# Performance work log

Hardware: AMD Instinct MI355X
Metric: run time of the kernel (lower is better)

Reference implementation:

```python
import jax, jax.numpy as jnp
import numpy as np
from jax import lax

COCO_80_TO_91 = [1,2,3,4,5,6,7,8,9,10,11,13,14,15,16,17,18,19,20,21,22,23,24,25,27,28,31,32,33,34,35,36,37,38,39,40,41,42,43,44,46,47,48,49,50,51,52,53,54,55,56,57,58,59,60,61,62,63,64,65,67,70,72,73,74,75,76,77,78,79,80,81,82,84,85,86,87,88,89,90]

CONF = 0.25      # self.confidence
IOU_THR = 0.7    # ultralytics NMS default
TOPK = 1000      # candidate cap before NMS
MAX_DET = 300    # ultralytics max_det default
MAX_WH = 7680.0  # per-class offset trick
IMG_SZ = 640.0   # yolov8 letterboxed input size


def setup_inputs() -> dict:
    key = jax.random.key(0)
    preds = jax.random.uniform(key, (32, 84, 8400), dtype=jnp.float32)
    return {"preds": preds}


def _nms_single(boxes, scores):
    """Greedy NMS on score-descending boxes [K,4] (class-offset xyxy). Returns keep mask [K]."""
    K = boxes.shape[0]
    area = (boxes[:, 2] - boxes[:, 0]) * (boxes[:, 3] - boxes[:, 1])  # [K]
    lt = jnp.maximum(boxes[:, None, :2], boxes[None, :, :2])          # [K,K,2]
    rb = jnp.minimum(boxes[:, None, 2:], boxes[None, :, 2:])
    wh = jnp.clip(rb - lt, 0.0)
    inter = wh[..., 0] * wh[..., 1]
    iou = inter / (area[:, None] + area[None, :] - inter + 1e-7)       # [K,K]
    idx = jnp.arange(K)
    sup = (iou > IOU_THR) & (idx[None, :] > idx[:, None])              # i suppresses later j

    def body(i, keep):
        return jnp.where(keep[i], keep & ~sup[i], keep)

    return lax.fori_loop(0, K, body, jnp.ones((K,), dtype=bool))


def reference(preds):
    # preds: [B, 84, N] -> [B, N, 84]
    p = jnp.transpose(preds, (0, 2, 1))
    box_xywh = p[..., :4] * IMG_SZ           # xywh in pixels on 640x640 canvas
    cls = p[..., 4:]                          # [B, N, 80]
    scores = jnp.max(cls, axis=-1)            # best-class confidence
    labels = jnp.argmax(cls, axis=-1)         # 0..79
    xy, wh = box_xywh[..., :2], box_xywh[..., 2:]
    xyxy = jnp.concatenate([xy - wh * 0.5, xy + wh * 0.5], axis=-1)  # decode

    # confidence filter + top-K candidate selection (score-descending)
    s_masked = jnp.where(scores > CONF, scores, -1.0)
    top_s, top_i = lax.top_k(s_masked, TOPK)                          # [B,TOPK]
    top_b = jnp.take_along_axis(xyxy, top_i[..., None], axis=1)      # [B,TOPK,4]
    top_l = jnp.take_along_axis(labels, top_i, axis=1)               # [B,TOPK]

    # per-class NMS via class offset
    off_b = top_b + (top_l.astype(top_b.dtype) * MAX_WH)[..., None]
    keep = jax.vmap(_nms_single)(off_b, top_s) & (top_s > CONF)

    # select final max_det detections, zero-pad invalid slots
    fin_s = jnp.where(keep, top_s, -1.0)
    out_s, out_i = lax.top_k(fin_s, MAX_DET)                          # [B,MAX_DET]
    out_b = jnp.take_along_axis(top_b, out_i[..., None], axis=1)
    out_l = jnp.take_along_axis(top_l, out_i, axis=1)
    valid = out_s > CONF
    boxes = jnp.where(valid[..., None], out_b, 0.0)
    scores_out = jnp.where(valid, out_s, 0.0)
    mapped = jnp.asarray(COCO_80_TO_91, dtype=jnp.int64)[out_l]       # COCO 80 -> 91 ids
    labels_out = jnp.where(valid, mapped, 0)
    return boxes, scores_out, labels_out
```

## Files before the change

### kernel.cpp

```cpp
#include <hip/hip_runtime.h>
#include <stdint.h>

typedef unsigned long long u64;
typedef unsigned int u32;

#define BATCH 32
#define NCH 84
#define NA 8400
#define NCLS 80
#define TOPK 1000
#define MAXDET 300
#define CONF 0.25f
#define IOU_T 0.7f
#define MAX_WH 7680.0f
#define IMG_SZ 640.0f
#define NT 1024
#define KPT 9
#define NCOPY 8
#define HPAD 260
#define DTILE 256

__device__ __constant__ float coco_map_f[NCLS] = {
    1,2,3,4,5,6,7,8,9,10,11,13,14,15,16,17,18,19,20,21,22,23,24,25,27,28,
    31,32,33,34,35,36,37,38,39,40,41,42,43,44,46,47,48,49,50,51,52,53,54,
    55,56,57,58,59,60,61,62,63,64,65,67,70,72,73,74,75,76,77,78,79,80,81,
    82,84,85,86,87,88,89,90};

__device__ inline u64 shflx64(u64 v, int m) {
    int lo = __shfl_xor((int)(u32)(v & 0xFFFFFFFFull), m, 64);
    int hi = __shfl_xor((int)(u32)(v >> 32), m, 64);
    return ((u64)(u32)hi << 32) | (u32)lo;
}

__global__ __launch_bounds__(256)
void decode_kernel(const float* __restrict__ preds,
                   u64* __restrict__ keys,
                   float4* __restrict__ boxes) {
    const int b = blockIdx.y;
    const int t = threadIdx.x;
    const int w = t >> 6, l = t & 63;
    const int wa = blockIdx.x * DTILE + w * 64;
    const int a = wa + l;
    const float* p = preds + (size_t)b * NCH * NA;

    __shared__ float stage[4][16][64];

    float bx = 0.f, by = 0.f, bw = 0.f, bh = 0.f;
    float best = -1.0f;
    int bl = 0;

    const int rsel = l >> 4;
    const int c4 = (l & 15) * 4;
    const int col = wa + c4;

    for (int chunk = 0; chunk < 6; ++chunk) {
        const int r0 = chunk * 16;
        const int nq = (chunk == 5) ? 1 : 4;
        for (int i = 0; i < nq; ++i) {
            int row = r0 + i * 4 + rsel;
            float4 v = (col < NA) ? *(const float4*)(p + (size_t)row * NA + col)
                                  : make_float4(0.f, 0.f, 0.f, 0.f);
            *(float4*)&stage[w][i * 4 + rsel][c4] = v;
        }
        __builtin_amdgcn_s_waitcnt(0xc07f);
        const int nr = (chunk == 5) ? 4 : 16;
        if (chunk == 0) {
            bx = stage[w][0][l]; by = stage[w][1][l];
            bw = stage[w][2][l]; bh = stage[w][3][l];
            best = stage[w][4][l]; bl = 0;
            for (int r = 5; r < 16; ++r) {
                float v = stage[w][r][l];
                int c = r - 4;
                bl = (v > best) ? c : bl;  best = fmaxf(v, best);
            }
        } else {
            for (int r = 0; r < nr; ++r) {
                float v = stage[w][r][l];
                int c = r0 + r - 4;
                bl = (v > best) ? c : bl;  best = fmaxf(v, best);
            }
        }
        __builtin_amdgcn_s_waitcnt(0xc07f);
    }

    if (a < NA) {
        float fx = bx * IMG_SZ, fy = by * IMG_SZ;
        float fw = bw * IMG_SZ, fh = bh * IMG_SZ;
        float hw = fw * 0.5f, hh = fh * 0.5f;
        boxes[(size_t)b * NA + a] = make_float4(fx - hw, fy - hh, fx + hw, fy + hh);
        float s = (best > CONF) ? best : -1.0f;
        u32 fb = __float_as_uint(s);
        u32 u = (fb & 0x80000000u) ? ~fb : (fb | 0x80000000u);
        keys[(size_t)b * NA + a] =
            ((u64)u << 21) | ((u64)(16383 - a) << 7) | (u64)bl;
    }
}

__global__ __launch_bounds__(NT, 4)
void fused_kernel(const u64* __restrict__ keys,
                  const float4* __restrict__ boxes,
                  float* __restrict__ out) {
    const int b = blockIdx.x;
    const int t = threadIdx.x;
    const int lane = t & 63, wid = t >> 6;

    __shared__ union {
        struct {
            u64 sk[2][NT];
            int hist[NCOPY * HPAD];
        } a;
        struct {
            u64 cmask2[NCLS][16];
        } bb;
        struct {
            float4 obox[NT];
            float  area[NT];
            unsigned short ranks[NCLS][64];
            int    cnt[NCLS];
            unsigned char cls[NT];
            unsigned char keep[NT];
        } c;
    } u_s;
    __shared__ int selB, selK, hselS, smax, scnt, cnt_s;
    __shared__ int wsum[16], woff[16], ktot_s;

    u64 kreg[KPT];
    const u64* kb = keys + (size_t)b * NA;
#pragma unroll
    for (int j = 0; j < KPT; ++j) {
        int i = t + j * NT;
        kreg[j] = (i < NA) ? kb[i] : 0ull;
    }

    u64 P = 0ull;
    int kk = TOPK;
    int nsel = 0;
    for (int d = 3; d >= 0; --d) {
        const int sh = 21 + 8 * d;
        __syncthreads();
        if (t == 0) { smax = -1; scnt = 0; }
        __syncthreads();
        u64 hmask = (~0ull) << (sh + 8);
        int dig[KPT];
        int mymax = -1;
#pragma unroll
        for (int j = 0; j < KPT; ++j) {
            bool act = (((kreg[j] ^ P) & hmask) == 0ull) && (kreg[j] != 0ull);
            dig[j] = act ? (int)((kreg[j] >> sh) & 255) : -1;
            mymax = max(mymax, dig[j]);
        }
#pragma unroll
        for (int off = 32; off; off >>= 1)
            mymax = max(mymax, __shfl_down(mymax, off, 64));
        if (lane == 0) atomicMax(&smax, mymax);
        __syncthreads();
        int maxb = smax;
        int myc = 0;
#pragma unroll
        for (int j = 0; j < KPT; ++j) myc += (dig[j] == maxb) ? 1 : 0;
#pragma unroll
        for (int off = 32; off; off >>= 1) myc += __shfl_down(myc, off, 64);
        if (lane == 0) atomicAdd(&scnt, myc);
        __syncthreads();
        int cm = scnt;
        if (cm >= kk) {
            P |= ((u64)maxb) << sh;
            nsel = TOPK - kk + cm;
            if (nsel <= NT) break;
            continue;
        }
        for (int i = t; i < NCOPY * HPAD; i += NT) u_s.a.hist[i] = 0;
        __syncthreads();
        int* myh = u_s.a.hist + (wid & (NCOPY - 1)) * HPAD;
#pragma unroll
        for (int j = 0; j < KPT; ++j)
            if (dig[j] >= 0) atomicAdd(&myh[dig[j]], 1);
        __syncthreads();
        if (t < 64) {
            int h0 = 0, h1 = 0, h2 = 0, h3 = 0;
            for (int c = 0; c < NCOPY; ++c) {
                const int* hp = u_s.a.hist + c * HPAD + 4 * t;
                h0 += hp[0]; h1 += hp[1]; h2 += hp[2]; h3 += hp[3];
            }
            int s = h0 + h1 + h2 + h3;
            int S = s;
            #pragma unroll
            for (int off = 1; off < 64; off <<= 1) {
                int o = __shfl_down(S, off, 64);
                if (t + off < 64) S += o;
            }
            int Snext = S - s;
            int c3 = Snext + h3, c2 = c3 + h2, c1 = c2 + h1, c0 = c1 + h0;
            int cand = -1, above = 0;
            if (c0 >= kk) {
                if      (c3 >= kk) { cand = 4 * t + 3; above = Snext; }
                else if (c2 >= kk) { cand = 4 * t + 2; above = c3; }
                else if (c1 >= kk) { cand = 4 * t + 1; above = c2; }
                else               { cand = 4 * t;     above = c1; }
            }
            int pc = (cand < 0) ? 0 : (((cand + 1) << 16) | (kk - above));
            #pragma unroll
            for (int off = 32; off; off >>= 1)
                pc = max(pc, __shfl_down(pc, off, 64));
            pc = __shfl(pc, 0, 64);
            int B = (pc >> 16) - 1;
            if (t == (B >> 2)) {
                int m4 = B & 3;
                selB = B;
                selK = pc & 0xFFFF;
                hselS = (m4 == 0) ? h0 : (m4 == 1) ? h1 : (m4 == 2) ? h2 : h3;
            }
        }
        __syncthreads();
        P |= ((u64)selB) << sh;
        kk = selK;
        nsel = TOPK - kk + hselS;
        if (nsel <= NT) break;
    }

    __syncthreads();
    if (t == 0) cnt_s = 0;
    __syncthreads();
#pragma unroll
    for (int j = 0; j < KPT; ++j) {
        bool p = (kreg[j] >= P);
        u64 m = __ballot(p);
        int base = 0;
        if (lane == 0) base = atomicAdd(&cnt_s, (int)__popcll(m));
        base = __shfl(base, 0, 64);
        if (p) {
            int pos = base + (int)__popcll(m & ((1ull << lane) - 1ull));
            if (pos < NT) u_s.a.sk[0][pos] = kreg[j];
        }
    }
    if (t < NT - nsel) u_s.a.sk[0][nsel + t] = 0ull;
    __syncthreads();

    u64 myk = u_s.a.sk[0][t];
    int buf = 1;
    for (int size = 2; size <= NT; size <<= 1) {
        bool up = ((t & size) == 0);
        for (int stride = size >> 1; stride; stride >>= 1) {
            u64 pk;
            if (stride >= 64) {
                u_s.a.sk[buf][t] = myk;
                __syncthreads();
                pk = u_s.a.sk[buf][t ^ stride];
                buf ^= 1;
            } else {
                pk = shflx64(myk, stride);
            }
            bool tlow = ((t & stride) == 0);
            u64 mn = (myk < pk) ? myk : pk;
            u64 mx = (myk < pk) ? pk : myk;
            myk = up ? (tlow ? mx : mn) : (tlow ? mn : mx);
        }
    }

    __syncthreads();
    for (int i = t; i < NCLS * 16; i += NT) ((u64*)u_s.bb.cmask2)[i] = 0ull;
    __syncthreads();

    int my_L = 0;
    float sj = -1.0f;
    float4 bx = make_float4(0.f, 0.f, 0.f, 0.f);
    if (t < TOPK) {
        int my_a = 16383 - (int)((myk >> 7) & 16383ull);
        my_L = (int)(myk & 127ull);
        bx = boxes[(size_t)b * NA + my_a];
        u32 u = (u32)(myk >> 21);
        u32 fb = (u & 0x80000000u) ? (u ^ 0x80000000u) : ~u;
        sj = __uint_as_float(fb);
        atomicOr(&u_s.bb.cmask2[my_L][t >> 6], 1ull << (t & 63));
    }
    __syncthreads();
    int r = 0, cntreg = 0;
    if (t < TOPK) {
        int w = t >> 6;
        r = __popcll(u_s.bb.cmask2[my_L][w] & ((1ull << (t & 63)) - 1ull));
        for (int q = 0; q < w; ++q) r += __popcll(u_s.bb.cmask2[my_L][q]);
    }
    if (t < NCLS) {
#pragma unroll
        for (int q = 0; q < 16; ++q) cntreg += __popcll(u_s.bb.cmask2[t][q]);
    }
    __syncthreads();

    float off = (float)my_L * MAX_WH;
    float ox0 = bx.x + off, oy0 = bx.y + off, ox1 = bx.z + off, oy1 = bx.w + off;
    float ar = (ox1 - ox0) * (oy1 - oy0);
    if (t < TOPK) {
        u_s.c.obox[t] = make_float4(ox0, oy0, ox1, oy1);
        u_s.c.area[t] = ar;
        u_s.c.cls[t]  = (unsigned char)my_L;
        if (r < 64) u_s.c.ranks[my_L][r] = (unsigned short)t;
    } else {
        u_s.c.cls[t] = 255;
    }
    u_s.c.keep[t] = 0;
    if (t < NCLS) u_s.c.cnt[t] = cntreg;
    __syncthreads();

    for (int jc = 0; jc < 5; ++jc) {
        const int cc = wid + 16 * jc;
        const int n = u_s.c.cnt[cc];
        if (n == 0) continue;
        if (n <= 64) {
            float4 bbx = make_float4(0.f, 0.f, 0.f, 0.f);
            float aa = 0.f;
            int rk = 0;
            if (lane < n) {
                rk  = u_s.c.ranks[cc][lane];
                bbx = u_s.c.obox[rk];
                aa  = u_s.c.area[rk];
            }
            u64 colm = 0ull;
            for (int i = 0; i < n; ++i) {
                float hx0 = __shfl(bbx.x, i, 64);
                float hy0 = __shfl(bbx.y, i, 64);
                float hx1 = __shfl(bbx.z, i, 64);
                float hy1 = __shfl(bbx.w, i, 64);
                float ha  = __shfl(aa, i, 64);
                float lx = fmaxf(hx0, bbx.x), ly = fmaxf(hy0, bbx.y);
                float rx = fminf(hx1, bbx.z), ry = fminf(hy1, bbx.w);
                float w = fmaxf(rx - lx, 0.0f);
                float h = fmaxf(ry - ly, 0.0f);
                float inter = w * h;
                float denom = ha + aa;
                denom = denom - inter;
                denom = denom + 1e-7f;
                bool s = (lane > i) && (lane < n) && (inter / denom > IOU_T);
                colm |= ((u64)s) << i;
            }
            u64 alive = (n >= 64) ? ~0ull : ((1ull << n) - 1ull);
            for (int i = 0; i < n; ++i) {
                if (!((alive >> i) & 1ull)) continue;
                alive &= ~__ballot((colm >> i) & 1ull);
            }
            if (lane < n) u_s.c.keep[rk] = (unsigned char)((alive >> lane) & 1ull);
        } else if (lane == 0) {
            u64 aliveW[16];
            for (int q = 0; q < 16; ++q) aliveW[q] = ~0ull;
            for (int i = 0; i < TOPK; ++i) {
                if (u_s.c.cls[i] != (unsigned char)cc) continue;
                if (!((aliveW[i >> 6] >> (i & 63)) & 1ull)) continue;
                float4 bi = u_s.c.obox[i];
                float ai = u_s.c.area[i];
                for (int jj = i + 1; jj < TOPK; ++jj) {
                    if (u_s.c.cls[jj] != (unsigned char)cc) continue;
                    if (!((aliveW[jj >> 6] >> (jj & 63)) & 1ull)) continue;
                    float4 bj = u_s.c.obox[jj];
                    float lx = fmaxf(bi.x, bj.x), ly = fmaxf(bi.y, bj.y);
                    float rx = fminf(bi.z, bj.z), ry = fminf(bi.w, bj.w);
                    float w = fmaxf(rx - lx, 0.0f);
                    float h = fmaxf(ry - ly, 0.0f);
                    float inter = w * h;
                    float denom = ai + u_s.c.area[jj];
                    denom = denom - inter;
                    denom = denom + 1e-7f;
                    if (inter / denom > IOU_T) aliveW[jj >> 6] &= ~(1ull << (jj & 63));
                }
            }
            for (int i = 0; i < TOPK; ++i)
                if (u_s.c.cls[i] == (unsigned char)cc)
                    u_s.c.keep[i] = (unsigned char)((aliveW[i >> 6] >> (i & 63)) & 1ull);
        }
    }
    __syncthreads();

    bool valid = (t < TOPK) && u_s.c.keep[t] && (sj > CONF);
    u64 m = __ballot(valid);
    if (lane == 0) wsum[wid] = (int)__popcll(m);
    __syncthreads();
    if (wid == 0) {
        int v = (lane < 16) ? wsum[lane] : 0;
        #pragma unroll
        for (int o = 1; o < 16; o <<= 1) {
            int x = __shfl_up(v, o, 64);
            if (lane >= o) v += x;
        }
        if (lane < 16) woff[lane] = v - wsum[lane];
        if (lane == 15) ktot_s = v;
    }
    __syncthreads();
    int ktot = ktot_s;
    int rank = woff[wid] + (int)__popcll(m & ((1ull << lane) - 1ull));

    float* out_boxes = out;
    float* out_scores = out + (size_t)BATCH * MAXDET * 4;
    float* out_labels = out + (size_t)BATCH * MAXDET * 5;
    if (valid && rank < MAXDET) {
        float* ob = out_boxes + ((size_t)b * MAXDET + rank) * 4;
        ob[0] = bx.x; ob[1] = bx.y; ob[2] = bx.z; ob[3] = bx.w;
        out_scores[(size_t)b * MAXDET + rank] = sj;
        out_labels[(size_t)b * MAXDET + rank] = coco_map_f[my_L];
    }
    if (t < MAXDET && t >= ktot) {
        float* ob = out_boxes + ((size_t)b * MAXDET + t) * 4;
        ob[0] = 0.0f; ob[1] = 0.0f; ob[2] = 0.0f; ob[3] = 0.0f;
        out_scores[(size_t)b * MAXDET + t] = 0.0f;
        out_labels[(size_t)b * MAXDET + t] = 0.0f;
    }
}

extern "C" void kernel_launch(void* const* d_in, const int* in_sizes, int n_in,
                              void* d_out, int out_size, void* d_ws, size_t ws_size,
                              hipStream_t stream) {
    const float* preds = (const float*)d_in[0];
    char* ws = (char*)d_ws;
    size_t off = 0;
    auto alloc = [&](size_t bytes) { char* p = ws + off; off += (bytes + 255) & ~(size_t)255; return p; };

    u64* keys     = (u64*)    alloc((size_t)BATCH * NA * 8);
    float4* boxes = (float4*) alloc((size_t)BATCH * NA * 16);
    float* out = (float*)d_out;

    dim3 dgrid((NA + DTILE - 1) / DTILE, BATCH);
    decode_kernel<<<dgrid, 256, 0, stream>>>(preds, keys, boxes);
    fused_kernel<<<BATCH, NT, 0, stream>>>(keys, boxes, out);
}
```

Baseline: 176.3 us.

## Simplify decode loads and cut barriers in radix-select passes

The decode kernel drops its LDS-staged float4 tile loads and reads each class channel directly with coalesced per-thread scalar loads. In the fused kernel, each radix-select pass now uses per-wave partial slots plus a 16-way reduction instead of shared atomics. This removes the reset barriers, and histogram zeroing moves earlier to overlap with the max pass. Digits are recomputed from registers rather than stored in an array, which lowers register pressure. The occupancy hint becomes an explicit waves-per-EU attribute, and the direct loads may issue more memory instructions than the float4 path.

After: 179.0 us. Within noise of the previous version (+1.5%).

```diff
diff --git a/kernel.cpp b/kernel.cpp
--- a/kernel.cpp
+++ b/kernel.cpp
@@ -18,7 +18,6 @@
 #define KPT 9
 #define NCOPY 8
 #define HPAD 260
-#define DTILE 256
 
 __device__ __constant__ float coco_map_f[NCLS] = {
     1,2,3,4,5,6,7,8,9,10,11,13,14,15,16,17,18,19,20,21,22,23,24,25,27,28,
@@ -37,53 +36,27 @@
                    u64* __restrict__ keys,
                    float4* __restrict__ boxes) {
     const int b = blockIdx.y;
-    const int t = threadIdx.x;
-    const int w = t >> 6, l = t & 63;
-    const int wa = blockIdx.x * DTILE + w * 64;
-    const int a = wa + l;
-    const float* p = preds + (size_t)b * NCH * NA;
-
-    __shared__ float stage[4][16][64];
-
-    float bx = 0.f, by = 0.f, bw = 0.f, bh = 0.f;
+    const int a = blockIdx.x * 256 + threadIdx.x;
+    const bool live = (a < NA);
+    const int ac = live ? a : (NA - 1);
+    const float* p = preds + (size_t)b * NCH * NA + ac;
+
+    float bx = p[0];
+    float by = p[(size_t)1 * NA];
+    float bw = p[(size_t)2 * NA];
+    float bh = p[(size_t)3 * NA];
+
+    const float* pc = p + (size_t)4 * NA;
     float best = -1.0f;
     int bl = 0;
-
-    const int rsel = l >> 4;
-    const int c4 = (l & 15) * 4;
-    const int col = wa + c4;
-
-    for (int chunk = 0; chunk < 6; ++chunk) {
-        const int r0 = chunk * 16;
-        const int nq = (chunk == 5) ? 1 : 4;
-        for (int i = 0; i < nq; ++i) {
-            int row = r0 + i * 4 + rsel;
-            float4 v = (col < NA) ? *(const float4*)(p + (size_t)row * NA + col)
-                                  : make_float4(0.f, 0.f, 0.f, 0.f);
-            *(float4*)&stage[w][i * 4 + rsel][c4] = v;
-        }
-        __builtin_amdgcn_s_waitcnt(0xc07f);
-        const int nr = (chunk == 5) ? 4 : 16;
-        if (chunk == 0) {
-            bx = stage[w][0][l]; by = stage[w][1][l];
-            bw = stage[w][2][l]; bh = stage[w][3][l];
-            best = stage[w][4][l]; bl = 0;
-            for (int r = 5; r < 16; ++r) {
-                float v = stage[w][r][l];
-                int c = r - 4;
-                bl = (v > best) ? c : bl;  best = fmaxf(v, best);
-            }
-        } else {
-            for (int r = 0; r < nr; ++r) {
-                float v = stage[w][r][l];
-                int c = r0 + r - 4;
-                bl = (v > best) ? c : bl;  best = fmaxf(v, best);
-            }
-        }
-        __builtin_amdgcn_s_waitcnt(0xc07f);
-    }
-
-    if (a < NA) {
+#pragma unroll 16
+    for (int r = 0; r < NCLS; ++r) {
+        float v = pc[(size_t)r * NA];
+        bl = (v > best) ? r : bl;
+        best = fmaxf(v, best);
+    }
+
+    if (live) {
         float fx = bx * IMG_SZ, fy = by * IMG_SZ;
         float fw = bw * IMG_SZ, fh = bh * IMG_SZ;
         float hw = fw * 0.5f, hh = fh * 0.5f;
@@ -96,10 +69,11 @@
     }
 }
 
-__global__ __launch_bounds__(NT, 4)
-void fused_kernel(const u64* __restrict__ keys,
-                  const float4* __restrict__ boxes,
-                  float* __restrict__ out) {
+__global__ void __launch_bounds__(NT)
+__attribute__((amdgpu_waves_per_eu(4, 4)))
+fused_kernel(const u64* __restrict__ keys,
+             const float4* __restrict__ boxes,
+             float* __restrict__ out) {
     const int b = blockIdx.x;
     const int t = threadIdx.x;
     const int lane = t & 63, wid = t >> 6;
@@ -121,7 +95,7 @@
             unsigned char keep[NT];
         } c;
     } u_s;
-    __shared__ int selB, selK, hselS, smax, scnt, cnt_s;
+    __shared__ int selB, selK, hselS, cnt_s;
     __shared__ int wsum[16], woff[16], ktot_s;
 
     u64 kreg[KPT];
@@ -137,44 +111,50 @@
     int nsel = 0;
     for (int d = 3; d >= 0; --d) {
         const int sh = 21 + 8 * d;
-        __syncthreads();
-        if (t == 0) { smax = -1; scnt = 0; }
-        __syncthreads();
-        u64 hmask = (~0ull) << (sh + 8);
-        int dig[KPT];
+        const u64 hmask = (~0ull) << (sh + 8);
         int mymax = -1;
 #pragma unroll
         for (int j = 0; j < KPT; ++j) {
             bool act = (((kreg[j] ^ P) & hmask) == 0ull) && (kreg[j] != 0ull);
-            dig[j] = act ? (int)((kreg[j] >> sh) & 255) : -1;
-            mymax = max(mymax, dig[j]);
+            int dg = act ? (int)((kreg[j] >> sh) & 255) : -1;
+            mymax = max(mymax, dg);
         }
 #pragma unroll
         for (int off = 32; off; off >>= 1)
             mymax = max(mymax, __shfl_down(mymax, off, 64));
-        if (lane == 0) atomicMax(&smax, mymax);
+        if (lane == 0) wsum[wid] = mymax;
+        for (int i = t; i < NCOPY * HPAD; i += NT) u_s.a.hist[i] = 0;
         __syncthreads();
-        int maxb = smax;
+        int maxb = wsum[0];
+#pragma unroll
+        for (int q = 1; q < 16; ++q) maxb = max(maxb, wsum[q]);
         int myc = 0;
 #pragma unroll
-        for (int j = 0; j < KPT; ++j) myc += (dig[j] == maxb) ? 1 : 0;
+        for (int j = 0; j < KPT; ++j) {
+            bool act = (((kreg[j] ^ P) & hmask) == 0ull) && (kreg[j] != 0ull);
+            int dg = act ? (int)((kreg[j] >> sh) & 255) : -1;
+            myc += (dg == maxb) ? 1 : 0;
+        }
 #pragma unroll
         for (int off = 32; off; off >>= 1) myc += __shfl_down(myc, off, 64);
-        if (lane == 0) atomicAdd(&scnt, myc);
+        if (lane == 0) woff[wid] = myc;
         __syncthreads();
-        int cm = scnt;
+        int cm = 0;
+#pragma unroll
+        for (int q = 0; q < 16; ++q) cm += woff[q];
         if (cm >= kk) {
             P |= ((u64)maxb) << sh;
             nsel = TOPK - kk + cm;
             if (nsel <= NT) break;
             continue;
         }
-        for (int i = t; i < NCOPY * HPAD; i += NT) u_s.a.hist[i] = 0;
-        __syncthreads();
         int* myh = u_s.a.hist + (wid & (NCOPY - 1)) * HPAD;
 #pragma unroll
-        for (int j = 0; j < KPT; ++j)
-            if (dig[j] >= 0) atomicAdd(&myh[dig[j]], 1);
+        for (int j = 0; j < KPT; ++j) {
+            bool act = (((kreg[j] ^ P) & hmask) == 0ull) && (kreg[j] != 0ull);
+            int dg = act ? (int)((kreg[j] >> sh) & 255) : -1;
+            if (dg >= 0) atomicAdd(&myh[dg], 1);
+        }
         __syncthreads();
         if (t < 64) {
             int h0 = 0, h1 = 0, h2 = 0, h3 = 0;
@@ -415,7 +395,7 @@
     float4* boxes = (float4*) alloc((size_t)BATCH * NA * 16);
     float* out = (float*)d_out;
 
-    dim3 dgrid((NA + DTILE - 1) / DTILE, BATCH);
+    dim3 dgrid((NA + 255) / 256, BATCH);
     decode_kernel<<<dgrid, 256, 0, stream>>>(preds, keys, boxes);
     fused_kernel<<<BATCH, NT, 0, stream>>>(keys, boxes, out);
 }
```
